# Optimization experiments

Hardware: AMD Instinct MI355X
Metric: run time of the kernel (lower is better)

Reference implementation:

```python
import jax, jax.numpy as jnp
import numpy as np

H = 512  # hidden_dim


def _lstm_layer(x, W_ih, W_hh, b_ih, b_hh):
    # x: [B, T, D]; W_ih: [4H, D]; W_hh: [4H, H]; biases: [4H]
    B, T, _ = x.shape
    Hh = W_hh.shape[1]
    # Precompute input contribution as one big GEMM: [B, T, 4H]
    xg = jnp.einsum('btd,gd->btg', x, W_ih) + b_ih + b_hh

    def step(carry, xt):
        h, c = carry
        gates = xt + h @ W_hh.T  # [B, 4H]
        i, f, g, o = jnp.split(gates, 4, axis=-1)  # PyTorch gate order: i, f, g, o
        i = jax.nn.sigmoid(i)
        f = jax.nn.sigmoid(f)
        g = jnp.tanh(g)
        o = jax.nn.sigmoid(o)
        c = f * c + i * g
        h = o * jnp.tanh(c)
        return (h, c), h

    h0 = jnp.zeros((B, Hh), x.dtype)
    (_, _), hs = jax.lax.scan(step, (h0, h0), jnp.swapaxes(xg, 0, 1))  # hs: [T, B, H]
    return jnp.swapaxes(hs, 0, 1)  # [B, T, H]


def setup_inputs() -> dict:
    key = jax.random.key(0)
    ks = jax.random.split(key, 11)
    s = 1.0 / np.sqrt(H)
    D_in, D_out = 3, 3
    inp = {
        'x': jax.random.normal(ks[0], (256, 512, D_in), dtype=jnp.float32),
        'W_ih0': jax.random.uniform(ks[1], (4 * H, D_in), jnp.float32, -s, s),
        'W_hh0': jax.random.uniform(ks[2], (4 * H, H), jnp.float32, -s, s),
        'b_ih0': jax.random.uniform(ks[3], (4 * H,), jnp.float32, -s, s),
        'b_hh0': jax.random.uniform(ks[4], (4 * H,), jnp.float32, -s, s),
        'W_ih1': jax.random.uniform(ks[5], (4 * H, H), jnp.float32, -s, s),
        'W_hh1': jax.random.uniform(ks[6], (4 * H, H), jnp.float32, -s, s),
        'b_ih1': jax.random.uniform(ks[7], (4 * H,), jnp.float32, -s, s),
        'b_hh1': jax.random.uniform(ks[8], (4 * H,), jnp.float32, -s, s),
        'W_fc': jax.random.uniform(ks[9], (D_out, H), jnp.float32, -s, s),
        'b_fc': jax.random.uniform(ks[10], (D_out,), jnp.float32, -s, s),
    }
    return inp


def reference(x, W_ih0, W_hh0, b_ih0, b_hh0, W_ih1, W_hh1, b_ih1, b_hh1, W_fc, b_fc):
    h = _lstm_layer(x, W_ih0, W_hh0, b_ih0, b_hh0)
    h = _lstm_layer(h, W_ih1, W_hh1, b_ih1, b_hh1)
    return h @ W_fc.T + b_fc  # [B, T, output_dim]
```

## Files before the change

### kernel.cpp

```cpp
#include <hip/hip_runtime.h>
#include <stdint.h>

#define SEQT   512
#define HID    512
#define GRPS   8
#define SLICES 32
#define GB     32
#define NTHR   512

typedef __attribute__((ext_vector_type(8))) short bf16x8;
typedef __attribute__((ext_vector_type(4))) float f32x4;

#define WMAT_ELEMS 1048576
#define WS_H_OFF   12582912
#define HBUF_ELEMS 16384
#define HARR_ELEMS 262144
#define WS_BAR_OFF 14680064
#define BAR_STRIDE 640
#define SMEM_BYTES 153600

__device__ __forceinline__ unsigned short f2bf(float x){
    unsigned int u = __float_as_uint(x);
    u = (u + 0x7fffu + ((u >> 16) & 1u)) >> 16;
    return (unsigned short)u;
}
__device__ __forceinline__ float bf2f(unsigned short h){
    return __uint_as_float(((unsigned int)h) << 16);
}
__device__ __forceinline__ float sigm(float v){ return 1.0f / (1.0f + __expf(-v)); }
__device__ __forceinline__ float tanh_(float v){
    float e = __expf(2.0f * v);
    return (e - 1.0f) / (e + 1.0f);
}

__global__ void prep_weights(const float* __restrict__ W0,
                             const float* __restrict__ W1,
                             const float* __restrict__ W2,
                             short* __restrict__ wp)
{
    const int mat = blockIdx.y;
    const float* src = (mat == 0) ? W0 : ((mat == 1) ? W1 : W2);
    short* dh = wp + (size_t)mat * (2 * WMAT_ELEMS);
    short* dl = dh + WMAT_ELEMS;
    const int jg = blockIdx.x;
    const int j = jg >> 2, g = jg & 3;
    for (int rep = 0; rep < 2; ++rep){
        int task = rep * NTHR + (int)threadIdx.x;
        int kt = task >> 6, l = task & 63;
        int row = g * 512 + j * 16 + (l & 15);
        int k0  = kt * 32 + ((l >> 4) & 3) * 8;
        const float* s = src + (size_t)row * HID + k0;
        bf16x8 vh, vl;
        #pragma unroll
        for (int e = 0; e < 8; ++e){
            float v = s[e];
            unsigned short hb = f2bf(v);
            vh[e] = (short)hb;
            vl[e] = (short)f2bf(v - bf2f(hb));
        }
        size_t o = ((size_t)(jg * 16 + kt) * 64 + l) * 8;
        *(bf16x8*)(dh + o) = vh;
        *(bf16x8*)(dl + o) = vl;
    }
}

__global__ void __launch_bounds__(NTHR, 2)
lstm2_mfma(const float* __restrict__ x,
           const float* __restrict__ Wih0,
           const float* __restrict__ bih0, const float* __restrict__ bhh0,
           const float* __restrict__ bih1, const float* __restrict__ bhh1,
           const float* __restrict__ Wfc,  const float* __restrict__ bfc,
           float* __restrict__ out, char* __restrict__ ws)
{
    extern __shared__ char smem[];
    short* lh1h = (short*)smem;
    short* lh1l = lh1h + 16384;
    short* lh2h = lh1l + 16384;
    short* lh2l = lh2h + 16384;
    float* g1   = (float*)(smem + 131072);
    float* g2   = g1 + 2048;
    float* fcb  = g2 + 2048;

    const short* Wp  = (const short*)ws;
    const short* W0h = Wp;                      const short* W0l = Wp + WMAT_ELEMS;
    const short* W1h = Wp + 2 * WMAT_ELEMS;     const short* W1l = Wp + 3 * WMAT_ELEMS;
    const short* W2h = Wp + 4 * WMAT_ELEMS;     const short* W2l = Wp + 5 * WMAT_ELEMS;
    short* h1h_ws = (short*)(ws + WS_H_OFF);
    short* h1l_ws = h1h_ws + HARR_ELEMS;
    short* h2h_ws = h1h_ws + 2 * HARR_ELEMS;
    short* h2l_ws = h1h_ws + 3 * HARR_ELEMS;
    unsigned int* bar = (unsigned int*)(ws + WS_BAR_OFF);

    const int tid = threadIdx.x;
    const int wg  = blockIdx.x;
    const int grp = wg >> 5;
    const int j   = wg & 31;

    const int wv = tid >> 6, lane = tid & 63;
    const int g  = wv >> 1, kh = wv & 1;
    const int ablk = (j * 4 + g) * 16;

    const int q  = tid >> 5, b = tid & 31;
    const int qg = j * 16 + q;
    const int nn = b >> 4, bl = b & 15;
    const int eidx = (((qg >> 5) * 2 + nn) * 64 + ((qg >> 3) & 3) * 16 + bl) * 8 + (qg & 7);

    float bias1[4], bias2[4], wxr[4][3];
    #pragma unroll
    for (int gg = 0; gg < 4; ++gg){
        int row = gg * 512 + qg;
        bias1[gg] = bih0[row] + bhh0[row];
        bias2[gg] = bih1[row] + bhh1[row];
        wxr[gg][0] = Wih0[row * 3 + 0];
        wxr[gg][1] = Wih0[row * 3 + 1];
        wxr[gg][2] = Wih0[row * 3 + 2];
    }
    const float wf0 = Wfc[qg], wf1 = Wfc[512 + qg], wf2 = Wfc[1024 + qg];

    float c1 = 0.f, c2 = 0.f;

    for (int p = 0; p <= SEQT; ++p){
        const int rs1 = (p + 1) & 1;
        const int rs2 = p & 1;

        {
            const float4* s0 = (const float4*)(h1h_ws + (rs1 * GRPS + grp) * HBUF_ELEMS);
            const float4* s1 = (const float4*)(h1l_ws + (rs1 * GRPS + grp) * HBUF_ELEMS);
            const float4* s2 = (const float4*)(h2h_ws + (rs2 * GRPS + grp) * HBUF_ELEMS);
            const float4* s3 = (const float4*)(h2l_ws + (rs2 * GRPS + grp) * HBUF_ELEMS);
            float4* d0 = (float4*)lh1h; float4* d1 = (float4*)lh1l;
            float4* d2 = (float4*)lh2h; float4* d3 = (float4*)lh2l;
            #pragma unroll
            for (int r = 0; r < 4; ++r){
                int i4 = r * NTHR + tid;
                d0[i4] = s0[i4]; d1[i4] = s1[i4]; d2[i4] = s2[i4]; d3[i4] = s3[i4];
            }
        }
        __syncthreads();

        f32x4 acc1[2] = {{0.f,0.f,0.f,0.f},{0.f,0.f,0.f,0.f}};
        f32x4 acc2[2] = {{0.f,0.f,0.f,0.f},{0.f,0.f,0.f,0.f}};
        #pragma unroll 2
        for (int ks = 0; ks < 8; ++ks){
            const int kt = kh * 8 + ks;
            const size_t ao = ((size_t)(ablk + kt) * 64 + lane) * 8;
            bf16x8 a0h = *(const bf16x8*)(W0h + ao);
            bf16x8 a0l = *(const bf16x8*)(W0l + ao);
            bf16x8 a1h = *(const bf16x8*)(W1h + ao);
            bf16x8 a1l = *(const bf16x8*)(W1l + ao);
            bf16x8 a2h = *(const bf16x8*)(W2h + ao);
            bf16x8 a2l = *(const bf16x8*)(W2l + ao);
            #pragma unroll
            for (int n = 0; n < 2; ++n){
                const int bo = ((kt * 2 + n) * 64 + lane) * 8;
                bf16x8 b1h = *(const bf16x8*)(lh1h + bo);
                bf16x8 b1l = *(const bf16x8*)(lh1l + bo);
                bf16x8 b2h = *(const bf16x8*)(lh2h + bo);
                bf16x8 b2l = *(const bf16x8*)(lh2l + bo);
                acc1[n] = __builtin_amdgcn_mfma_f32_16x16x32_bf16(a0h, b1h, acc1[n], 0, 0, 0);
                acc1[n] = __builtin_amdgcn_mfma_f32_16x16x32_bf16(a0h, b1l, acc1[n], 0, 0, 0);
                acc1[n] = __builtin_amdgcn_mfma_f32_16x16x32_bf16(a0l, b1h, acc1[n], 0, 0, 0);
                acc2[n] = __builtin_amdgcn_mfma_f32_16x16x32_bf16(a1h, b1h, acc2[n], 0, 0, 0);
                acc2[n] = __builtin_amdgcn_mfma_f32_16x16x32_bf16(a1h, b1l, acc2[n], 0, 0, 0);
                acc2[n] = __builtin_amdgcn_mfma_f32_16x16x32_bf16(a1l, b1h, acc2[n], 0, 0, 0);
                acc2[n] = __builtin_amdgcn_mfma_f32_16x16x32_bf16(a2h, b2h, acc2[n], 0, 0, 0);
                acc2[n] = __builtin_amdgcn_mfma_f32_16x16x32_bf16(a2h, b2l, acc2[n], 0, 0, 0);
                acc2[n] = __builtin_amdgcn_mfma_f32_16x16x32_bf16(a2l, b2h, acc2[n], 0, 0, 0);
            }
        }

        if (kh == 0){
            #pragma unroll
            for (int n = 0; n < 2; ++n)
                #pragma unroll
                for (int r = 0; r < 4; ++r){
                    int qrow = (lane >> 4) * 4 + r;
                    int idx = ((g * 2 + n) * 16 + qrow) * 16 + (lane & 15);
                    g1[idx] = acc1[n][r];
                    g2[idx] = acc2[n][r];
                }
        }
        __syncthreads();
        if (kh == 1){
            #pragma unroll
            for (int n = 0; n < 2; ++n)
                #pragma unroll
                for (int r = 0; r < 4; ++r){
                    int qrow = (lane >> 4) * 4 + r;
                    int idx = ((g * 2 + n) * 16 + qrow) * 16 + (lane & 15);
                    g1[idx] += acc1[n][r];
                    g2[idx] += acc2[n][r];
                }
        }
        __syncthreads();

        if (p < SEQT){
            float gt0 = bias1[0] + g1[((0 * 2 + nn) * 16 + q) * 16 + bl];
            float gt1 = bias1[1] + g1[((1 * 2 + nn) * 16 + q) * 16 + bl];
            float gt2 = bias1[2] + g1[((2 * 2 + nn) * 16 + q) * 16 + bl];
            float gt3 = bias1[3] + g1[((3 * 2 + nn) * 16 + q) * 16 + bl];
            const float* xp = x + ((size_t)(grp * GB + b) * SEQT + p) * 3;
            float x0 = xp[0], x1 = xp[1], x2 = xp[2];
            gt0 += wxr[0][0] * x0 + wxr[0][1] * x1 + wxr[0][2] * x2;
            gt1 += wxr[1][0] * x0 + wxr[1][1] * x1 + wxr[1][2] * x2;
            gt2 += wxr[2][0] * x0 + wxr[2][1] * x1 + wxr[2][2] * x2;
            gt3 += wxr[3][0] * x0 + wxr[3][1] * x1 + wxr[3][2] * x2;
            float ii = sigm(gt0), ff = sigm(gt1), gv = tanh_(gt2), oo = sigm(gt3);
            c1 = ff * c1 + ii * gv;
            float h = oo * tanh_(c1);
            unsigned short hb = f2bf(h);
            unsigned short lb = f2bf(h - bf2f(hb));
            int base = ((p & 1) * GRPS + grp) * HBUF_ELEMS;
            h1h_ws[base + eidx] = (short)hb;
            h1l_ws[base + eidx] = (short)lb;
        }

        if (p >= 1){
            float gt0 = bias2[0] + g2[((0 * 2 + nn) * 16 + q) * 16 + bl];
            float gt1 = bias2[1] + g2[((1 * 2 + nn) * 16 + q) * 16 + bl];
            float gt2 = bias2[2] + g2[((2 * 2 + nn) * 16 + q) * 16 + bl];
            float gt3 = bias2[3] + g2[((3 * 2 + nn) * 16 + q) * 16 + bl];
            float ii = sigm(gt0), ff = sigm(gt1), gv = tanh_(gt2), oo = sigm(gt3);
            c2 = ff * c2 + ii * gv;
            float h = oo * tanh_(c2);
            unsigned short hb = f2bf(h);
            unsigned short lb = f2bf(h - bf2f(hb));
            int base = (((p - 1) & 1) * GRPS + grp) * HBUF_ELEMS;
            h2h_ws[base + eidx] = (short)hb;
            h2l_ws[base + eidx] = (short)lb;
            fcb[0 * 512 + tid] = wf0 * h;
            fcb[1 * 512 + tid] = wf1 * h;
            fcb[2 * 512 + tid] = wf2 * h;
        }
        __syncthreads();
        if (p >= 1 && tid < 96){
            int d = tid >> 5, bb = tid & 31;
            float s = 0.f;
            #pragma unroll
            for (int qq = 0; qq < 16; ++qq) s += fcb[d * 512 + qq * 32 + bb];
            if (j == 0) s += bfc[d];
            atomicAdd(out + ((size_t)(grp * GB + bb) * SEQT + (p - 1)) * 3 + d, s);
        }

        if (tid == 0){
            unsigned int* c = bar + grp * BAR_STRIDE + p;
            __hip_atomic_fetch_add(c, 1u, __ATOMIC_RELEASE, __HIP_MEMORY_SCOPE_AGENT);
            while (__hip_atomic_load(c, __ATOMIC_RELAXED, __HIP_MEMORY_SCOPE_AGENT) < (unsigned)SLICES) {}
            __builtin_amdgcn_fence(__ATOMIC_ACQUIRE, "agent");
        }
        __syncthreads();
    }
}

extern "C" void kernel_launch(void* const* d_in, const int* in_sizes, int n_in,
                              void* d_out, int out_size, void* d_ws, size_t ws_size,
                              hipStream_t stream)
{
    (void)in_sizes; (void)n_in; (void)ws_size;

    const float* x    = (const float*)d_in[0];
    const float* Wih0 = (const float*)d_in[1];
    const float* Whh0 = (const float*)d_in[2];
    const float* bih0 = (const float*)d_in[3];
    const float* bhh0 = (const float*)d_in[4];
    const float* Wih1 = (const float*)d_in[5];
    const float* Whh1 = (const float*)d_in[6];
    const float* bih1 = (const float*)d_in[7];
    const float* bhh1 = (const float*)d_in[8];
    const float* Wfc  = (const float*)d_in[9];
    const float* bfc  = (const float*)d_in[10];
    float* out = (float*)d_out;
    char*  ws  = (char*)d_ws;

    hipMemsetAsync(ws + WS_H_OFF, 0, 4 * HARR_ELEMS * sizeof(short), stream);
    hipMemsetAsync(ws + WS_BAR_OFF, 0, GRPS * BAR_STRIDE * sizeof(unsigned int), stream);
    hipMemsetAsync(d_out, 0, (size_t)out_size * sizeof(float), stream);

    prep_weights<<<dim3(128, 3), NTHR, 0, stream>>>(Whh0, Wih1, Whh1, (short*)ws);

    hipFuncSetAttribute((const void*)lstm2_mfma,
                        hipFuncAttributeMaxDynamicSharedMemorySize, SMEM_BYTES);

    void* args[] = { (void*)&x, (void*)&Wih0, (void*)&bih0, (void*)&bhh0,
                     (void*)&bih1, (void*)&bhh1, (void*)&Wfc, (void*)&bfc,
                     (void*)&out, (void*)&ws };
    hipLaunchCooperativeKernel((const void*)lstm2_mfma, dim3(GRPS * SLICES), dim3(NTHR),
                               args, SMEM_BYTES, stream);
}
```

Before: 11.38 ms.

## Keep high weight halves in registers and pack h hi/lo exchange into dwords

```diff
diff --git a/kernel.cpp b/kernel.cpp
--- a/kernel.cpp
+++ b/kernel.cpp
@@ -10,11 +10,11 @@
 
 typedef __attribute__((ext_vector_type(8))) short bf16x8;
 typedef __attribute__((ext_vector_type(4))) float f32x4;
+typedef unsigned int uint32;
 
 #define WMAT_ELEMS 1048576
 #define WS_H_OFF   12582912
 #define HBUF_ELEMS 16384
-#define HARR_ELEMS 262144
 #define WS_BAR_OFF 14680064
 #define BAR_STRIDE 640
 #define SMEM_BYTES 153600
@@ -85,10 +85,8 @@
     const short* W0h = Wp;                      const short* W0l = Wp + WMAT_ELEMS;
     const short* W1h = Wp + 2 * WMAT_ELEMS;     const short* W1l = Wp + 3 * WMAT_ELEMS;
     const short* W2h = Wp + 4 * WMAT_ELEMS;     const short* W2l = Wp + 5 * WMAT_ELEMS;
-    short* h1h_ws = (short*)(ws + WS_H_OFF);
-    short* h1l_ws = h1h_ws + HARR_ELEMS;
-    short* h2h_ws = h1h_ws + 2 * HARR_ELEMS;
-    short* h2l_ws = h1h_ws + 3 * HARR_ELEMS;
+    uint32* h1p_ws = (uint32*)(ws + WS_H_OFF);
+    uint32* h2p_ws = h1p_ws + 2 * GRPS * HBUF_ELEMS;
     unsigned int* bar = (unsigned int*)(ws + WS_BAR_OFF);
 
     const int tid = threadIdx.x;
@@ -117,6 +115,16 @@
     }
     const float wf0 = Wfc[qg], wf1 = Wfc[512 + qg], wf2 = Wfc[1024 + qg];
 
+    bf16x8 w0h[8], w1h[8], w2h[8];
+    #pragma unroll
+    for (int ks = 0; ks < 8; ++ks){
+        const int kt = kh * 8 + ks;
+        const size_t ao = ((size_t)(ablk + kt) * 64 + lane) * 8;
+        w0h[ks] = *(const bf16x8*)(W0h + ao);
+        w1h[ks] = *(const bf16x8*)(W1h + ao);
+        w2h[ks] = *(const bf16x8*)(W2h + ao);
+    }
+
     float c1 = 0.f, c2 = 0.f;
 
     for (int p = 0; p <= SEQT; ++p){
@@ -124,31 +132,45 @@
         const int rs2 = p & 1;
 
         {
-            const float4* s0 = (const float4*)(h1h_ws + (rs1 * GRPS + grp) * HBUF_ELEMS);
-            const float4* s1 = (const float4*)(h1l_ws + (rs1 * GRPS + grp) * HBUF_ELEMS);
-            const float4* s2 = (const float4*)(h2h_ws + (rs2 * GRPS + grp) * HBUF_ELEMS);
-            const float4* s3 = (const float4*)(h2l_ws + (rs2 * GRPS + grp) * HBUF_ELEMS);
-            float4* d0 = (float4*)lh1h; float4* d1 = (float4*)lh1l;
-            float4* d2 = (float4*)lh2h; float4* d3 = (float4*)lh2l;
-            #pragma unroll
-            for (int r = 0; r < 4; ++r){
-                int i4 = r * NTHR + tid;
-                d0[i4] = s0[i4]; d1[i4] = s1[i4]; d2[i4] = s2[i4]; d3[i4] = s3[i4];
+            const unsigned long long* s1 =
+                (const unsigned long long*)(h1p_ws + (rs1 * GRPS + grp) * HBUF_ELEMS);
+            const unsigned long long* s2 =
+                (const unsigned long long*)(h2p_ws + (rs2 * GRPS + grp) * HBUF_ELEMS);
+            uint32* d1h = (uint32*)lh1h; uint32* d1l = (uint32*)lh1l;
+            uint32* d2h = (uint32*)lh2h; uint32* d2l = (uint32*)lh2l;
+
+            unsigned long long v[16];
+            #pragma unroll
+            for (int c = 0; c < 16; ++c)
+                v[c] = __hip_atomic_load(s1 + c * 512 + tid,
+                                         __ATOMIC_RELAXED, __HIP_MEMORY_SCOPE_AGENT);
+            #pragma unroll
+            for (int c = 0; c < 16; ++c){
+                uint32 a = (uint32)v[c], bo_ = (uint32)(v[c] >> 32);
+                d1h[c * 512 + tid] = __builtin_amdgcn_perm(bo_, a, 0x05040100u);
+                d1l[c * 512 + tid] = __builtin_amdgcn_perm(bo_, a, 0x07060302u);
+            }
+            #pragma unroll
+            for (int c = 0; c < 16; ++c)
+                v[c] = __hip_atomic_load(s2 + c * 512 + tid,
+                                         __ATOMIC_RELAXED, __HIP_MEMORY_SCOPE_AGENT);
+            #pragma unroll
+            for (int c = 0; c < 16; ++c){
+                uint32 a = (uint32)v[c], bo_ = (uint32)(v[c] >> 32);
+                d2h[c * 512 + tid] = __builtin_amdgcn_perm(bo_, a, 0x05040100u);
+                d2l[c * 512 + tid] = __builtin_amdgcn_perm(bo_, a, 0x07060302u);
             }
         }
         __syncthreads();
 
         f32x4 acc1[2] = {{0.f,0.f,0.f,0.f},{0.f,0.f,0.f,0.f}};
         f32x4 acc2[2] = {{0.f,0.f,0.f,0.f},{0.f,0.f,0.f,0.f}};
-        #pragma unroll 2
+        #pragma unroll
         for (int ks = 0; ks < 8; ++ks){
             const int kt = kh * 8 + ks;
             const size_t ao = ((size_t)(ablk + kt) * 64 + lane) * 8;
-            bf16x8 a0h = *(const bf16x8*)(W0h + ao);
             bf16x8 a0l = *(const bf16x8*)(W0l + ao);
-            bf16x8 a1h = *(const bf16x8*)(W1h + ao);
             bf16x8 a1l = *(const bf16x8*)(W1l + ao);
-            bf16x8 a2h = *(const bf16x8*)(W2h + ao);
             bf16x8 a2l = *(const bf16x8*)(W2l + ao);
             #pragma unroll
             for (int n = 0; n < 2; ++n){
@@ -157,15 +179,15 @@
                 bf16x8 b1l = *(const bf16x8*)(lh1l + bo);
                 bf16x8 b2h = *(const bf16x8*)(lh2h + bo);
                 bf16x8 b2l = *(const bf16x8*)(lh2l + bo);
-                acc1[n] = __builtin_amdgcn_mfma_f32_16x16x32_bf16(a0h, b1h, acc1[n], 0, 0, 0);
-                acc1[n] = __builtin_amdgcn_mfma_f32_16x16x32_bf16(a0h, b1l, acc1[n], 0, 0, 0);
-                acc1[n] = __builtin_amdgcn_mfma_f32_16x16x32_bf16(a0l, b1h, acc1[n], 0, 0, 0);
-                acc2[n] = __builtin_amdgcn_mfma_f32_16x16x32_bf16(a1h, b1h, acc2[n], 0, 0, 0);
-                acc2[n] = __builtin_amdgcn_mfma_f32_16x16x32_bf16(a1h, b1l, acc2[n], 0, 0, 0);
-                acc2[n] = __builtin_amdgcn_mfma_f32_16x16x32_bf16(a1l, b1h, acc2[n], 0, 0, 0);
-                acc2[n] = __builtin_amdgcn_mfma_f32_16x16x32_bf16(a2h, b2h, acc2[n], 0, 0, 0);
-                acc2[n] = __builtin_amdgcn_mfma_f32_16x16x32_bf16(a2h, b2l, acc2[n], 0, 0, 0);
-                acc2[n] = __builtin_amdgcn_mfma_f32_16x16x32_bf16(a2l, b2h, acc2[n], 0, 0, 0);
+                acc1[n] = __builtin_amdgcn_mfma_f32_16x16x32_bf16(w0h[ks], b1h, acc1[n], 0, 0, 0);
+                acc1[n] = __builtin_amdgcn_mfma_f32_16x16x32_bf16(w0h[ks], b1l, acc1[n], 0, 0, 0);
+                acc1[n] = __builtin_amdgcn_mfma_f32_16x16x32_bf16(a0l,     b1h, acc1[n], 0, 0, 0);
+                acc2[n] = __builtin_amdgcn_mfma_f32_16x16x32_bf16(w1h[ks], b1h, acc2[n], 0, 0, 0);
+                acc2[n] = __builtin_amdgcn_mfma_f32_16x16x32_bf16(w1h[ks], b1l, acc2[n], 0, 0, 0);
+                acc2[n] = __builtin_amdgcn_mfma_f32_16x16x32_bf16(a1l,     b1h, acc2[n], 0, 0, 0);
+                acc2[n] = __builtin_amdgcn_mfma_f32_16x16x32_bf16(w2h[ks], b2h, acc2[n], 0, 0, 0);
+                acc2[n] = __builtin_amdgcn_mfma_f32_16x16x32_bf16(w2h[ks], b2l, acc2[n], 0, 0, 0);
+                acc2[n] = __builtin_amdgcn_mfma_f32_16x16x32_bf16(a2l,     b2h, acc2[n], 0, 0, 0);
             }
         }
 
@@ -210,9 +232,9 @@
             float h = oo * tanh_(c1);
             unsigned short hb = f2bf(h);
             unsigned short lb = f2bf(h - bf2f(hb));
-            int base = ((p & 1) * GRPS + grp) * HBUF_ELEMS;
-            h1h_ws[base + eidx] = (short)hb;
-            h1l_ws[base + eidx] = (short)lb;
+            uint32 pv = (uint32)hb | ((uint32)lb << 16);
+            __hip_atomic_store(h1p_ws + ((p & 1) * GRPS + grp) * HBUF_ELEMS + eidx, pv,
+                               __ATOMIC_RELAXED, __HIP_MEMORY_SCOPE_AGENT);
         }
 
         if (p >= 1){
@@ -225,9 +247,9 @@
             float h = oo * tanh_(c2);
             unsigned short hb = f2bf(h);
             unsigned short lb = f2bf(h - bf2f(hb));
-            int base = (((p - 1) & 1) * GRPS + grp) * HBUF_ELEMS;
-            h2h_ws[base + eidx] = (short)hb;
-            h2l_ws[base + eidx] = (short)lb;
+            uint32 pv = (uint32)hb | ((uint32)lb << 16);
+            __hip_atomic_store(h2p_ws + (((p - 1) & 1) * GRPS + grp) * HBUF_ELEMS + eidx, pv,
+                               __ATOMIC_RELAXED, __HIP_MEMORY_SCOPE_AGENT);
             fcb[0 * 512 + tid] = wf0 * h;
             fcb[1 * 512 + tid] = wf1 * h;
             fcb[2 * 512 + tid] = wf2 * h;
@@ -246,7 +268,6 @@
             unsigned int* c = bar + grp * BAR_STRIDE + p;
             __hip_atomic_fetch_add(c, 1u, __ATOMIC_RELEASE, __HIP_MEMORY_SCOPE_AGENT);
             while (__hip_atomic_load(c, __ATOMIC_RELAXED, __HIP_MEMORY_SCOPE_AGENT) < (unsigned)SLICES) {}
-            __builtin_amdgcn_fence(__ATOMIC_ACQUIRE, "agent");
         }
         __syncthreads();
     }
@@ -272,8 +293,7 @@
     float* out = (float*)d_out;
     char*  ws  = (char*)d_ws;
 
-    hipMemsetAsync(ws + WS_H_OFF, 0, 4 * HARR_ELEMS * sizeof(short), stream);
-    hipMemsetAsync(ws + WS_BAR_OFF, 0, GRPS * BAR_STRIDE * sizeof(unsigned int), stream);
+    hipMemsetAsync(ws + WS_H_OFF, 0, (WS_BAR_OFF - WS_H_OFF) + GRPS * BAR_STRIDE * sizeof(unsigned int), stream);
     hipMemsetAsync(d_out, 0, (size_t)out_size * sizeof(float), stream);
 
     prep_weights<<<dim3(128, 3), NTHR, 0, stream>>>(Whh0, Wih1, Whh1, (short*)ws);
```

Measured after the change: 13.14 ms. +15.4%, slower.
